# Performance work log

Measured on AMD Instinct MI355X. Metric: run time of the kernel, lower is better.

## Reference

```python
import jax, jax.numpy as jnp
import numpy as np

BRANCH, VOCAB, FFN, BATCH = 8, 256, 1024, 16384
LN_EPS = 1e-5


def setup_inputs() -> dict:
    key = jax.random.key(0)
    ks = jax.random.split(key, 7)
    x = jax.random.normal(ks[0], (BATCH, BRANCH, VOCAB), dtype=jnp.float32)
    U1 = 0.01 * jax.random.normal(ks[1], (BRANCH, VOCAB, FFN), dtype=jnp.float32)
    b1 = 0.01 * jax.random.normal(ks[2], (BRANCH, FFN), dtype=jnp.float32)
    U2 = 0.01 * jax.random.normal(ks[3], (BRANCH, FFN, VOCAB), dtype=jnp.float32)
    b2 = 0.01 * jax.random.normal(ks[4], (BRANCH, VOCAB), dtype=jnp.float32)
    ln_w = jnp.ones((VOCAB,), dtype=jnp.float32)
    ln_b = jnp.zeros((VOCAB,), dtype=jnp.float32)
    return {"x": x, "U1": U1, "b1": b1, "U2": U2, "b2": b2, "ln_w": ln_w, "ln_b": ln_b}


def _layernorm(h, w, b):
    mu = jnp.mean(h, axis=-1, keepdims=True)
    var = jnp.var(h, axis=-1, keepdims=True)
    return (h - mu) * jax.lax.rsqrt(var + LN_EPS) * w + b


def reference(x, U1, b1, U2, b2, ln_w, ln_b):
    # x: (B, N, D); branch-wise batched GEMMs via einsum (avoids explicit permutes)
    skip = x
    h = jnp.einsum('bnd,nde->bne', x, U1) + b1        # (B, N, FFN)
    h = jax.nn.gelu(h, approximate=False)
    h = jnp.einsum('bne,ned->bnd', h, U2) + b2        # (B, N, VOCAB)
    h = _layernorm(h, ln_w, ln_b)
    h = jax.nn.gelu(h, approximate=False)
    out = skip + h
    return out.reshape(BATCH, 1, BRANCH * VOCAB)
```

## Files before the change

kernel.cpp:

```cpp
#include <hip/hip_runtime.h>
#include <hip/hip_bf16.h>

#define NBR   8
#define DV    256
#define FF    1024
#define RT    64
#define NCH   32
#define NROWS 16384

#define L_B1 0
#define L_B2 32768
#define L_HS 65536
#define LDS_BYTES 69632

using bf16x8 = __attribute__((ext_vector_type(8))) short;
using f32x4  = __attribute__((ext_vector_type(4))) float;

__device__ __forceinline__ unsigned short f2bf(float f) {
    unsigned int u = __builtin_bit_cast(unsigned int, f);
    unsigned int r = (u + 0x7fffu + ((u >> 16) & 1u)) >> 16;
    return (unsigned short)r;
}
__device__ __forceinline__ float gelu_fast(float x) {
    float x2 = x * x;
    float z  = x * fmaf(x2, -0.1029434959f, -2.3022078770f);
    float e  = __builtin_amdgcn_exp2f(z);
    return x * __builtin_amdgcn_rcpf(1.0f + e);
}

#define GLL(gsrc, ldst) __builtin_amdgcn_global_load_lds((const unsigned int*)(gsrc), (unsigned int*)(ldst), 16, 0, 0)
#define MFMA16 __builtin_amdgcn_mfma_f32_16x16x32_bf16

__global__ void prep_weights(const float* __restrict__ U1, const float* __restrict__ U2,
                             unsigned short* __restrict__ w1img, unsigned short* __restrict__ w2img)
{
    const int b = blockIdx.x;
    const int n = b >> 5, cch = b & 31;
    const int tid = threadIdx.x;
    char* img1 = (char*)w1img + ((size_t)b << 14);
    char* img2 = (char*)w2img + ((size_t)b << 14);
    const float* U1n = U1 + (size_t)n * DV * FF;
    const float* U2n = U2 + (size_t)n * FF * DV;
    #pragma unroll
    for (int e = 0; e < 4; ++e) {
        int p = tid + e * 256;
        int kkg = p >> 5, nn = p & 31;
        bf16x8 h;
        #pragma unroll
        for (int j = 0; j < 8; ++j)
            h[j] = (short)f2bf(U1n[(size_t)(kkg * 8 + j) * FF + cch * 32 + nn]);
        *(bf16x8*)(img1 + kkg * 512 + nn * 16) = h;
    }
    #pragma unroll
    for (int e = 0; e < 4; ++e) {
        int p = tid + e * 256;
        int qq = p >> 8, nn = p & 255;
        bf16x8 h;
        #pragma unroll
        for (int j = 0; j < 8; ++j)
            h[j] = (short)f2bf(U2n[(size_t)(cch * 32 + qq * 8 + j) * DV + nn]);
        *(bf16x8*)(img2 + qq * 4096 + nn * 16) = h;
    }
}

__global__ __launch_bounds__(512, 4)
void belayer_main(const float* __restrict__ x,
                  const unsigned short* __restrict__ w1img,
                  const unsigned short* __restrict__ w2img,
                  const float* __restrict__ b1g, const float* __restrict__ b2g,
                  const float* __restrict__ lnw, const float* __restrict__ lnb,
                  float* __restrict__ out)
{
    __shared__ __align__(16) char LDS[LDS_BYTES];
    const int tid  = threadIdx.x;
    const int lane = tid & 63;
    const int wave = tid >> 6;
    const int q = lane >> 4, c = lane & 15;
    const int n    = blockIdx.x & 7;
    const int tile = blockIdx.x >> 3;
    const int row0 = tile * RT;
    const int rowg   = wave >> 1;
    const int colsel = wave & 1;

    const char* g1base = (const char*)w1img + ((size_t)(n * NCH) << 14) + (wave << 11) + lane * 16;
    const char* g2base = (const char*)w2img + ((size_t)(n * NCH) << 14) + (wave << 11) + lane * 16;
    char* l1base = LDS + L_B1 + (wave << 11);
    char* l2base = LDS + L_B2 + (wave << 11);

#define STAGE1(T) do { const char* g_ = g1base + ((size_t)(T) << 14); \
        char* l_ = l1base + (((T) & 1) << 14); GLL(g_, l_); GLL(g_ + 1024, l_ + 1024); } while (0)
#define STAGE2(T) do { const char* g_ = g2base + ((size_t)(T) << 14); \
        char* l_ = l2base + (((T) & 1) << 14); GLL(g_, l_); GLL(g_ + 1024, l_ + 1024); } while (0)

    STAGE1(0); STAGE2(0);

    bf16x8 A[8];
    {
        const float* src = x + (((size_t)(row0 + rowg * 16 + c)) * NBR + n) * DV + q * 8;
        #pragma unroll
        for (int ks = 0; ks < 8; ++ks) {
            f32x4 v0 = *(const f32x4*)(src + ks * 32);
            f32x4 v1 = *(const f32x4*)(src + ks * 32 + 4);
            bf16x8 h;
            h[0] = (short)f2bf(v0[0]); h[1] = (short)f2bf(v0[1]);
            h[2] = (short)f2bf(v0[2]); h[3] = (short)f2bf(v0[3]);
            h[4] = (short)f2bf(v1[0]); h[5] = (short)f2bf(v1[1]);
            h[6] = (short)f2bf(v1[2]); h[7] = (short)f2bf(v1[3]);
            A[ks] = h;
        }
    }

    const unsigned aB1 = (unsigned)(q * 512 + (colsel * 16 + c) * 16);
    const unsigned aB2 = (unsigned)(q * 4096 + (colsel * 128 + c) * 16);
    const unsigned aH  = (unsigned)(q * 1024 + (rowg * 16 + c) * 16);
    unsigned aW[4];
    #pragma unroll
    for (int r = 0; r < 4; ++r)
        aW[r] = (unsigned)((colsel * 2 + (c >> 3)) * 1024 + (rowg * 16 + q * 4 + r) * 16 + (c & 7) * 2);

    f32x4 acc2[8];
    #pragma unroll
    for (int i = 0; i < 8; ++i) acc2[i] = (f32x4){0.f, 0.f, 0.f, 0.f};

    __syncthreads();

    for (int t = 0; t < NCH; ++t) {
        const unsigned h1 = L_B1 + ((unsigned)(t & 1) << 14);
        const unsigned h2 = L_B2 + ((unsigned)(t & 1) << 14);

        if (t + 1 < NCH) STAGE1(t + 1);
        float b1v = b1g[n * FF + t * 32 + colsel * 16 + c];
        f32x4 acc1 = (f32x4){0.f, 0.f, 0.f, 0.f};
        #pragma unroll
        for (int ks = 0; ks < 8; ++ks) {
            bf16x8 b = *(const bf16x8*)(LDS + h1 + aB1 + ks * 2048);
            acc1 = MFMA16(A[ks], b, acc1, 0, 0, 0);
        }
        #pragma unroll
        for (int r = 0; r < 4; ++r) {
            float g = gelu_fast(acc1[r] + b1v);
            *(unsigned short*)(LDS + L_HS + aW[r]) = f2bf(g);
        }
        __syncthreads();

        if (t + 1 < NCH) STAGE2(t + 1);
        bf16x8 a = *(const bf16x8*)(LDS + L_HS + aH);
        #pragma unroll
        for (int cf = 0; cf < 8; ++cf) {
            bf16x8 b = *(const bf16x8*)(LDS + h2 + aB2 + cf * 256);
            acc2[cf] = MFMA16(a, b, acc2[cf], 0, 0, 0);
        }
        __syncthreads();
    }

    float b2v[8];
    #pragma unroll
    for (int cf = 0; cf < 8; ++cf) b2v[cf] = b2g[n * DV + colsel * 128 + cf * 16 + c];

    float s[4] = {0.f, 0.f, 0.f, 0.f}, sq[4] = {0.f, 0.f, 0.f, 0.f};
    #pragma unroll
    for (int cf = 0; cf < 8; ++cf)
        #pragma unroll
        for (int r = 0; r < 4; ++r) {
            float v = acc2[cf][r] + b2v[cf];
            acc2[cf][r] = v;
            s[r]  += v;
            sq[r] += v * v;
        }
    #pragma unroll
    for (int m = 1; m < 16; m <<= 1)
        #pragma unroll
        for (int r = 0; r < 4; ++r) {
            s[r]  += __shfl_xor(s[r],  m, 64);
            sq[r] += __shfl_xor(sq[r], m, 64);
        }
    float* Lred = (float*)(LDS + L_HS);
    if (c == 0) {
        #pragma unroll
        for (int r = 0; r < 4; ++r) {
            int row = rowg * 16 + q * 4 + r;
            Lred[colsel * 128 + row]      = s[r];
            Lred[colsel * 128 + 64 + row] = sq[r];
        }
    }
    __syncthreads();
    float mu[4], rs[4];
    #pragma unroll
    for (int r = 0; r < 4; ++r) {
        int row = rowg * 16 + q * 4 + r;
        float ssum = Lred[row] + Lred[128 + row];
        float qsum = Lred[64 + row] + Lred[192 + row];
        float m_ = ssum * (1.0f / 256.0f);
        float var = qsum * (1.0f / 256.0f) - m_ * m_;
        mu[r] = m_;
        rs[r] = rsqrtf(var + 1e-5f);
    }
    #pragma unroll
    for (int cf = 0; cf < 8; ++cf) {
        int col = colsel * 128 + cf * 16 + c;
        float lw = lnw[col];
        float lb = lnb[col];
        #pragma unroll
        for (int r = 0; r < 4; ++r) {
            int grow = row0 + rowg * 16 + q * 4 + r;
            float v = (acc2[cf][r] - mu[r]) * rs[r] * lw + lb;
            float g = gelu_fast(v);
            size_t oi = ((size_t)grow * NBR + n) * DV + col;
            out[oi] = x[oi] + g;
        }
    }
#undef STAGE1
#undef STAGE2
}

extern "C" void kernel_launch(void* const* d_in, const int* in_sizes, int n_in,
                              void* d_out, int out_size, void* d_ws, size_t ws_size,
                              hipStream_t stream) {
    const float* x   = (const float*)d_in[0];
    const float* U1  = (const float*)d_in[1];
    const float* b1  = (const float*)d_in[2];
    const float* U2  = (const float*)d_in[3];
    const float* b2  = (const float*)d_in[4];
    const float* lnw = (const float*)d_in[5];
    const float* lnb = (const float*)d_in[6];
    float* out = (float*)d_out;

    unsigned short* w1img = (unsigned short*)d_ws;
    unsigned short* w2img = w1img + (size_t)4 * 1024 * 1024 / 2;

    prep_weights<<<dim3(256), dim3(256), 0, stream>>>(U1, U2, w1img, w2img);
    belayer_main<<<dim3((NROWS / RT) * NBR), dim3(512), 0, stream>>>(x, w1img, w2img, b1, b2, lnw, lnb, out);
}
```

Measured before the change: 229.7 us.

## Load second-GEMM weights directly to registers and use 32x32 MFMA tiles

The second GEMM now reads its bf16 weight fragments straight from global memory into registers, using a reorganised weight image, instead of staging them through double-buffered LDS. It also switches from 16x16x32 to 32x32x16 MFMA with a 2x4 wave tiling. This roughly halves LDS use, which can allow more resident blocks, and removes one global-to-LDS stream and its LDS reads. The cost is exposed global-load latency inside the loop, because the register loads for the current chunk are issued without prefetch, plus more registers and a 32-lane shuffle reduction in the LayerNorm epilogue.

```diff
diff --git a/kernel.cpp b/kernel.cpp
--- a/kernel.cpp
+++ b/kernel.cpp
@@ -9,12 +9,12 @@
 #define NROWS 16384
 
 #define L_B1 0
-#define L_B2 32768
-#define L_HS 65536
-#define LDS_BYTES 69632
+#define L_HS 32768
+#define LDS_BYTES 36864
 
 using bf16x8 = __attribute__((ext_vector_type(8))) short;
 using f32x4  = __attribute__((ext_vector_type(4))) float;
+using f32x16 = __attribute__((ext_vector_type(16))) float;
 
 __device__ __forceinline__ unsigned short f2bf(float f) {
     unsigned int u = __builtin_bit_cast(unsigned int, f);
@@ -30,6 +30,7 @@
 
 #define GLL(gsrc, ldst) __builtin_amdgcn_global_load_lds((const unsigned int*)(gsrc), (unsigned int*)(ldst), 16, 0, 0)
 #define MFMA16 __builtin_amdgcn_mfma_f32_16x16x32_bf16
+#define MFMA32 __builtin_amdgcn_mfma_f32_32x32x16_bf16
 
 __global__ void prep_weights(const float* __restrict__ U1, const float* __restrict__ U2,
                              unsigned short* __restrict__ w1img, unsigned short* __restrict__ w2img)
@@ -54,12 +55,12 @@
     #pragma unroll
     for (int e = 0; e < 4; ++e) {
         int p = tid + e * 256;
-        int qq = p >> 8, nn = p & 255;
+        int s = p >> 9, ct = (p >> 6) & 7, l = p & 63;
         bf16x8 h;
         #pragma unroll
         for (int j = 0; j < 8; ++j)
-            h[j] = (short)f2bf(U2n[(size_t)(cch * 32 + qq * 8 + j) * DV + nn]);
-        *(bf16x8*)(img2 + qq * 4096 + nn * 16) = h;
+            h[j] = (short)f2bf(U2n[(size_t)(cch * 32 + s * 16 + (l >> 5) * 8 + j) * DV + ct * 32 + (l & 31)]);
+        *(bf16x8*)(img2 + (p << 4)) = h;
     }
 }
 
@@ -76,23 +77,23 @@
     const int lane = tid & 63;
     const int wave = tid >> 6;
     const int q = lane >> 4, c = lane & 15;
+    const int hi = lane >> 5, c32 = lane & 31;
     const int n    = blockIdx.x & 7;
     const int tile = blockIdx.x >> 3;
     const int row0 = tile * RT;
-    const int rowg   = wave >> 1;
-    const int colsel = wave & 1;
+    const int rowg    = wave >> 1;
+    const int colsel  = wave & 1;
+    const int rowg2   = wave >> 2;
+    const int colpair = wave & 3;
 
     const char* g1base = (const char*)w1img + ((size_t)(n * NCH) << 14) + (wave << 11) + lane * 16;
-    const char* g2base = (const char*)w2img + ((size_t)(n * NCH) << 14) + (wave << 11) + lane * 16;
+    const char* g2img  = (const char*)w2img + ((size_t)(n * NCH) << 14) + lane * 16;
     char* l1base = LDS + L_B1 + (wave << 11);
-    char* l2base = LDS + L_B2 + (wave << 11);
 
 #define STAGE1(T) do { const char* g_ = g1base + ((size_t)(T) << 14); \
         char* l_ = l1base + (((T) & 1) << 14); GLL(g_, l_); GLL(g_ + 1024, l_ + 1024); } while (0)
-#define STAGE2(T) do { const char* g_ = g2base + ((size_t)(T) << 14); \
-        char* l_ = l2base + (((T) & 1) << 14); GLL(g_, l_); GLL(g_ + 1024, l_ + 1024); } while (0)
-
-    STAGE1(0); STAGE2(0);
+
+    STAGE1(0);
 
     bf16x8 A[8];
     {
@@ -111,23 +112,29 @@
     }
 
     const unsigned aB1 = (unsigned)(q * 512 + (colsel * 16 + c) * 16);
-    const unsigned aB2 = (unsigned)(q * 4096 + (colsel * 128 + c) * 16);
-    const unsigned aH  = (unsigned)(q * 1024 + (rowg * 16 + c) * 16);
     unsigned aW[4];
     #pragma unroll
     for (int r = 0; r < 4; ++r)
-        aW[r] = (unsigned)((colsel * 2 + (c >> 3)) * 1024 + (rowg * 16 + q * 4 + r) * 16 + (c & 7) * 2);
-
-    f32x4 acc2[8];
-    #pragma unroll
-    for (int i = 0; i < 8; ++i) acc2[i] = (f32x4){0.f, 0.f, 0.f, 0.f};
+        aW[r] = (unsigned)(((colsel * 2 + (c >> 3)) * 64 + rowg * 16 + q * 4 + r) * 16 + (c & 7) * 2);
+    const unsigned aH = (unsigned)((hi * 64 + rowg2 * 32 + c32) * 16);
+
+    f32x16 acc2[2];
+    #pragma unroll
+    for (int i = 0; i < 2; ++i)
+        #pragma unroll
+        for (int j = 0; j < 16; ++j) acc2[i][j] = 0.f;
 
     __syncthreads();
 
     for (int t = 0; t < NCH; ++t) {
         const unsigned h1 = L_B1 + ((unsigned)(t & 1) << 14);
-        const unsigned h2 = L_B2 + ((unsigned)(t & 1) << 14);
-
+
+        bf16x8 B2f[2][2];
+        #pragma unroll
+        for (int s = 0; s < 2; ++s)
+            #pragma unroll
+            for (int ti = 0; ti < 2; ++ti)
+                B2f[s][ti] = *(const bf16x8*)(g2img + ((size_t)t << 14) + ((s * 8 + colpair * 2 + ti) << 10));
         if (t + 1 < NCH) STAGE1(t + 1);
         float b1v = b1g[n * FF + t * 32 + colsel * 16 + c];
         f32x4 acc1 = (f32x4){0.f, 0.f, 0.f, 0.f};
@@ -143,74 +150,70 @@
         }
         __syncthreads();
 
-        if (t + 1 < NCH) STAGE2(t + 1);
-        bf16x8 a = *(const bf16x8*)(LDS + L_HS + aH);
-        #pragma unroll
-        for (int cf = 0; cf < 8; ++cf) {
-            bf16x8 b = *(const bf16x8*)(LDS + h2 + aB2 + cf * 256);
-            acc2[cf] = MFMA16(a, b, acc2[cf], 0, 0, 0);
+        #pragma unroll
+        for (int s = 0; s < 2; ++s) {
+            bf16x8 a = *(const bf16x8*)(LDS + L_HS + aH + s * 2048);
+            acc2[0] = MFMA32(a, B2f[s][0], acc2[0], 0, 0, 0);
+            acc2[1] = MFMA32(a, B2f[s][1], acc2[1], 0, 0, 0);
         }
         __syncthreads();
     }
 
-    float b2v[8];
-    #pragma unroll
-    for (int cf = 0; cf < 8; ++cf) b2v[cf] = b2g[n * DV + colsel * 128 + cf * 16 + c];
-
-    float s[4] = {0.f, 0.f, 0.f, 0.f}, sq[4] = {0.f, 0.f, 0.f, 0.f};
-    #pragma unroll
-    for (int cf = 0; cf < 8; ++cf)
-        #pragma unroll
-        for (int r = 0; r < 4; ++r) {
-            float v = acc2[cf][r] + b2v[cf];
-            acc2[cf][r] = v;
-            s[r]  += v;
-            sq[r] += v * v;
-        }
-    #pragma unroll
-    for (int m = 1; m < 16; m <<= 1)
-        #pragma unroll
-        for (int r = 0; r < 4; ++r) {
-            s[r]  += __shfl_xor(s[r],  m, 64);
-            sq[r] += __shfl_xor(sq[r], m, 64);
-        }
-    float* Lred = (float*)(LDS + L_HS);
-    if (c == 0) {
-        #pragma unroll
-        for (int r = 0; r < 4; ++r) {
-            int row = rowg * 16 + q * 4 + r;
-            Lred[colsel * 128 + row]      = s[r];
-            Lred[colsel * 128 + 64 + row] = sq[r];
+    float b2v[2], lwv[2], lbv[2];
+    #pragma unroll
+    for (int ti = 0; ti < 2; ++ti) {
+        int col = colpair * 64 + ti * 32 + c32;
+        b2v[ti] = b2g[n * DV + col];
+        lwv[ti] = lnw[col];
+        lbv[ti] = lnb[col];
+    }
+    float s[16], sq[16];
+    #pragma unroll
+    for (int reg = 0; reg < 16; ++reg) {
+        float v0 = acc2[0][reg] + b2v[0];
+        float v1 = acc2[1][reg] + b2v[1];
+        acc2[0][reg] = v0; acc2[1][reg] = v1;
+        s[reg]  = v0 + v1;
+        sq[reg] = v0 * v0 + v1 * v1;
+    }
+    #pragma unroll
+    for (int m = 1; m < 32; m <<= 1)
+        #pragma unroll
+        for (int reg = 0; reg < 16; ++reg) {
+            s[reg]  += __shfl_xor(s[reg],  m, 64);
+            sq[reg] += __shfl_xor(sq[reg], m, 64);
+        }
+    float* Lred = (float*)(LDS + L_B1);
+    if (c32 == 0) {
+        #pragma unroll
+        for (int reg = 0; reg < 16; ++reg) {
+            int ro = rowg2 * 32 + (reg & 3) + 8 * (reg >> 2) + 4 * hi;
+            Lred[ro * 4 + colpair]       = s[reg];
+            Lred[256 + ro * 4 + colpair] = sq[reg];
         }
     }
     __syncthreads();
-    float mu[4], rs[4];
-    #pragma unroll
-    for (int r = 0; r < 4; ++r) {
-        int row = rowg * 16 + q * 4 + r;
-        float ssum = Lred[row] + Lred[128 + row];
-        float qsum = Lred[64 + row] + Lred[192 + row];
-        float m_ = ssum * (1.0f / 256.0f);
-        float var = qsum * (1.0f / 256.0f) - m_ * m_;
-        mu[r] = m_;
-        rs[r] = rsqrtf(var + 1e-5f);
-    }
-    #pragma unroll
-    for (int cf = 0; cf < 8; ++cf) {
-        int col = colsel * 128 + cf * 16 + c;
-        float lw = lnw[col];
-        float lb = lnb[col];
-        #pragma unroll
-        for (int r = 0; r < 4; ++r) {
-            int grow = row0 + rowg * 16 + q * 4 + r;
-            float v = (acc2[cf][r] - mu[r]) * rs[r] * lw + lb;
+    #pragma unroll
+    for (int reg = 0; reg < 16; ++reg) {
+        int rowloc = (reg & 3) + 8 * (reg >> 2) + 4 * hi;
+        int ro = rowg2 * 32 + rowloc;
+        f32x4 sv = *(const f32x4*)(Lred + ro * 4);
+        f32x4 qv = *(const f32x4*)(Lred + 256 + ro * 4);
+        float ssum = sv[0] + sv[1] + sv[2] + sv[3];
+        float qsum = qv[0] + qv[1] + qv[2] + qv[3];
+        float mu = ssum * (1.0f / 256.0f);
+        float var = qsum * (1.0f / 256.0f) - mu * mu;
+        float rs = rsqrtf(var + 1e-5f);
+        int grow = row0 + ro;
+        #pragma unroll
+        for (int ti = 0; ti < 2; ++ti) {
+            float v = (acc2[ti][reg] - mu) * rs * lwv[ti] + lbv[ti];
             float g = gelu_fast(v);
-            size_t oi = ((size_t)grow * NBR + n) * DV + col;
+            size_t oi = ((size_t)grow * NBR + n) * DV + colpair * 64 + ti * 32 + c32;
             out[oi] = x[oi] + g;
         }
     }
 #undef STAGE1
-#undef STAGE2
 }
 
 extern "C" void kernel_launch(void* const* d_in, const int* in_sizes, int n_in,
```

After: 257.0 us. +11.9%, slower.

## Load second-GEMM weights directly into registers with 2x4 wave tiling, dropping LDS staging

Applied to the files above, without the earlier changes.

Second-GEMM weight fragments are now read straight from global memory into registers in a pre-swizzled MFMA fragment layout, removing the double-buffered LDS staging for U2. The waves are retiled into 2 row groups by 4 column groups, with each wave computing 32 rows by 64 columns. This halves the per-MFMA LDS reads of the hidden activation and cuts LDS use to about 36 KB, which could raise occupancy. In exchange, global load latency for the B2 fragments now sits on the critical path of every chunk, since they are loaded at the top of each iteration, and the layernorm reduction is reworked for four column groups.

```diff
diff --git a/kernel.cpp b/kernel.cpp
--- a/kernel.cpp
+++ b/kernel.cpp
@@ -9,9 +9,8 @@
 #define NROWS 16384
 
 #define L_B1 0
-#define L_B2 32768
-#define L_HS 65536
-#define LDS_BYTES 69632
+#define L_HS 32768
+#define LDS_BYTES 36864
 
 using bf16x8 = __attribute__((ext_vector_type(8))) short;
 using f32x4  = __attribute__((ext_vector_type(4))) float;
@@ -54,12 +53,12 @@
     #pragma unroll
     for (int e = 0; e < 4; ++e) {
         int p = tid + e * 256;
-        int qq = p >> 8, nn = p & 255;
+        int cfg = p >> 6, l = p & 63;
         bf16x8 h;
         #pragma unroll
         for (int j = 0; j < 8; ++j)
-            h[j] = (short)f2bf(U2n[(size_t)(cch * 32 + qq * 8 + j) * DV + nn]);
-        *(bf16x8*)(img2 + qq * 4096 + nn * 16) = h;
+            h[j] = (short)f2bf(U2n[(size_t)(cch * 32 + (l >> 4) * 8 + j) * DV + cfg * 16 + (l & 15)]);
+        *(bf16x8*)(img2 + (p << 4)) = h;
     }
 }
 
@@ -81,18 +80,17 @@
     const int row0 = tile * RT;
     const int rowg   = wave >> 1;
     const int colsel = wave & 1;
+    const int rowg2  = wave >> 2;
+    const int colg2  = wave & 3;
 
     const char* g1base = (const char*)w1img + ((size_t)(n * NCH) << 14) + (wave << 11) + lane * 16;
-    const char* g2base = (const char*)w2img + ((size_t)(n * NCH) << 14) + (wave << 11) + lane * 16;
+    const char* g2img  = (const char*)w2img + ((size_t)(n * NCH) << 14) + (colg2 << 12) + lane * 16;
     char* l1base = LDS + L_B1 + (wave << 11);
-    char* l2base = LDS + L_B2 + (wave << 11);
 
 #define STAGE1(T) do { const char* g_ = g1base + ((size_t)(T) << 14); \
         char* l_ = l1base + (((T) & 1) << 14); GLL(g_, l_); GLL(g_ + 1024, l_ + 1024); } while (0)
-#define STAGE2(T) do { const char* g_ = g2base + ((size_t)(T) << 14); \
-        char* l_ = l2base + (((T) & 1) << 14); GLL(g_, l_); GLL(g_ + 1024, l_ + 1024); } while (0)
-
-    STAGE1(0); STAGE2(0);
+
+    STAGE1(0);
 
     bf16x8 A[8];
     {
@@ -111,23 +109,27 @@
     }
 
     const unsigned aB1 = (unsigned)(q * 512 + (colsel * 16 + c) * 16);
-    const unsigned aB2 = (unsigned)(q * 4096 + (colsel * 128 + c) * 16);
-    const unsigned aH  = (unsigned)(q * 1024 + (rowg * 16 + c) * 16);
     unsigned aW[4];
     #pragma unroll
     for (int r = 0; r < 4; ++r)
-        aW[r] = (unsigned)((colsel * 2 + (c >> 3)) * 1024 + (rowg * 16 + q * 4 + r) * 16 + (c & 7) * 2);
-
-    f32x4 acc2[8];
-    #pragma unroll
-    for (int i = 0; i < 8; ++i) acc2[i] = (f32x4){0.f, 0.f, 0.f, 0.f};
+        aW[r] = (unsigned)(((colsel * 2 + (c >> 3)) * 64 + rowg * 16 + q * 4 + r) * 16 + (c & 7) * 2);
+    const unsigned aH = (unsigned)((q * 64 + rowg2 * 32 + c) * 16);
+
+    f32x4 acc2[2][4];
+    #pragma unroll
+    for (int i = 0; i < 2; ++i)
+        #pragma unroll
+        for (int j = 0; j < 4; ++j) acc2[i][j] = (f32x4){0.f, 0.f, 0.f, 0.f};
 
     __syncthreads();
 
     for (int t = 0; t < NCH; ++t) {
         const unsigned h1 = L_B1 + ((unsigned)(t & 1) << 14);
-        const unsigned h2 = L_B2 + ((unsigned)(t & 1) << 14);
-
+
+        bf16x8 B2f[4];
+        #pragma unroll
+        for (int cf = 0; cf < 4; ++cf)
+            B2f[cf] = *(const bf16x8*)(g2img + ((size_t)t << 14) + (cf << 10));
         if (t + 1 < NCH) STAGE1(t + 1);
         float b1v = b1g[n * FF + t * 32 + colsel * 16 + c];
         f32x4 acc1 = (f32x4){0.f, 0.f, 0.f, 0.f};
@@ -143,74 +145,89 @@
         }
         __syncthreads();
 
-        if (t + 1 < NCH) STAGE2(t + 1);
-        bf16x8 a = *(const bf16x8*)(LDS + L_HS + aH);
-        #pragma unroll
-        for (int cf = 0; cf < 8; ++cf) {
-            bf16x8 b = *(const bf16x8*)(LDS + h2 + aB2 + cf * 256);
-            acc2[cf] = MFMA16(a, b, acc2[cf], 0, 0, 0);
+        bf16x8 a0 = *(const bf16x8*)(LDS + L_HS + aH);
+        bf16x8 a1 = *(const bf16x8*)(LDS + L_HS + aH + 256);
+        #pragma unroll
+        for (int cf = 0; cf < 4; ++cf) {
+            acc2[0][cf] = MFMA16(a0, B2f[cf], acc2[0][cf], 0, 0, 0);
+            acc2[1][cf] = MFMA16(a1, B2f[cf], acc2[1][cf], 0, 0, 0);
         }
         __syncthreads();
     }
 
-    float b2v[8];
-    #pragma unroll
-    for (int cf = 0; cf < 8; ++cf) b2v[cf] = b2g[n * DV + colsel * 128 + cf * 16 + c];
-
-    float s[4] = {0.f, 0.f, 0.f, 0.f}, sq[4] = {0.f, 0.f, 0.f, 0.f};
-    #pragma unroll
-    for (int cf = 0; cf < 8; ++cf)
-        #pragma unroll
-        for (int r = 0; r < 4; ++r) {
-            float v = acc2[cf][r] + b2v[cf];
-            acc2[cf][r] = v;
-            s[r]  += v;
-            sq[r] += v * v;
-        }
+    float b2v[4];
+    #pragma unroll
+    for (int cf = 0; cf < 4; ++cf) b2v[cf] = b2g[n * DV + colg2 * 64 + cf * 16 + c];
+
+    float sA[2][4], sQ[2][4];
+    #pragma unroll
+    for (int rf = 0; rf < 2; ++rf)
+        #pragma unroll
+        for (int r = 0; r < 4; ++r) { sA[rf][r] = 0.f; sQ[rf][r] = 0.f; }
+    #pragma unroll
+    for (int rf = 0; rf < 2; ++rf)
+        #pragma unroll
+        for (int cf = 0; cf < 4; ++cf)
+            #pragma unroll
+            for (int r = 0; r < 4; ++r) {
+                float v = acc2[rf][cf][r] + b2v[cf];
+                acc2[rf][cf][r] = v;
+                sA[rf][r] += v;
+                sQ[rf][r] += v * v;
+            }
     #pragma unroll
     for (int m = 1; m < 16; m <<= 1)
         #pragma unroll
-        for (int r = 0; r < 4; ++r) {
-            s[r]  += __shfl_xor(s[r],  m, 64);
-            sq[r] += __shfl_xor(sq[r], m, 64);
-        }
+        for (int rf = 0; rf < 2; ++rf)
+            #pragma unroll
+            for (int r = 0; r < 4; ++r) {
+                sA[rf][r] += __shfl_xor(sA[rf][r], m, 64);
+                sQ[rf][r] += __shfl_xor(sQ[rf][r], m, 64);
+            }
     float* Lred = (float*)(LDS + L_HS);
     if (c == 0) {
         #pragma unroll
+        for (int rf = 0; rf < 2; ++rf)
+            #pragma unroll
+            for (int r = 0; r < 4; ++r) {
+                int row = rowg2 * 32 + rf * 16 + q * 4 + r;
+                Lred[row * 4 + colg2]       = sA[rf][r];
+                Lred[256 + row * 4 + colg2] = sQ[rf][r];
+            }
+    }
+    __syncthreads();
+    float mu[2][4], rs[2][4];
+    #pragma unroll
+    for (int rf = 0; rf < 2; ++rf)
+        #pragma unroll
         for (int r = 0; r < 4; ++r) {
-            int row = rowg * 16 + q * 4 + r;
-            Lred[colsel * 128 + row]      = s[r];
-            Lred[colsel * 128 + 64 + row] = sq[r];
-        }
-    }
-    __syncthreads();
-    float mu[4], rs[4];
-    #pragma unroll
-    for (int r = 0; r < 4; ++r) {
-        int row = rowg * 16 + q * 4 + r;
-        float ssum = Lred[row] + Lred[128 + row];
-        float qsum = Lred[64 + row] + Lred[192 + row];
-        float m_ = ssum * (1.0f / 256.0f);
-        float var = qsum * (1.0f / 256.0f) - m_ * m_;
-        mu[r] = m_;
-        rs[r] = rsqrtf(var + 1e-5f);
-    }
-    #pragma unroll
-    for (int cf = 0; cf < 8; ++cf) {
-        int col = colsel * 128 + cf * 16 + c;
+            int row = rowg2 * 32 + rf * 16 + q * 4 + r;
+            f32x4 sv = *(const f32x4*)(Lred + row * 4);
+            f32x4 qv = *(const f32x4*)(Lred + 256 + row * 4);
+            float ssum = sv[0] + sv[1] + sv[2] + sv[3];
+            float qsum = qv[0] + qv[1] + qv[2] + qv[3];
+            float m_ = ssum * (1.0f / 256.0f);
+            float var = qsum * (1.0f / 256.0f) - m_ * m_;
+            mu[rf][r] = m_;
+            rs[rf][r] = rsqrtf(var + 1e-5f);
+        }
+    #pragma unroll
+    for (int cf = 0; cf < 4; ++cf) {
+        int col = colg2 * 64 + cf * 16 + c;
         float lw = lnw[col];
         float lb = lnb[col];
         #pragma unroll
-        for (int r = 0; r < 4; ++r) {
-            int grow = row0 + rowg * 16 + q * 4 + r;
-            float v = (acc2[cf][r] - mu[r]) * rs[r] * lw + lb;
-            float g = gelu_fast(v);
-            size_t oi = ((size_t)grow * NBR + n) * DV + col;
-            out[oi] = x[oi] + g;
-        }
+        for (int rf = 0; rf < 2; ++rf)
+            #pragma unroll
+            for (int r = 0; r < 4; ++r) {
+                int row = rowg2 * 32 + rf * 16 + q * 4 + r;
+                float v = (acc2[rf][cf][r] - mu[rf][r]) * rs[rf][r] * lw + lb;
+                float g = gelu_fast(v);
+                size_t oi = ((size_t)(row0 + row) * NBR + n) * DV + col;
+                out[oi] = x[oi] + g;
+            }
     }
 #undef STAGE1
-#undef STAGE2
 }
 
 extern "C" void kernel_launch(void* const* d_in, const int* in_sizes, int n_in,
```

New measurement: 236.1 us. 1.03x slower.
